# Kernel optimization log

Measured on AMD Instinct MI355X. Metric: run time of the kernel, lower is better.

## Reference

```python
import jax, jax.numpy as jnp
import numpy as np

FACTOR = 5  # sampling factor from __init__


def setup_inputs() -> dict:
    key = jax.random.key(0)
    k1, k2, k3, k4 = jax.random.split(key, 4)
    B, L, H, D = 4, 2048, 8, 64
    S = min(FACTOR * int(np.ceil(np.log(L))), L)  # U_part = 40
    return {
        "queries": jax.random.normal(k1, (B, L, H, D), jnp.float32),
        "keys": jax.random.normal(k2, (B, L, H, D), jnp.float32),
        "values": jax.random.normal(k3, (B, L, H, D), jnp.float32),
        "index_sample": jax.random.randint(k4, (L, S), 0, L, jnp.int32),
    }


def reference(queries, keys, values, index_sample):
    B, L_Q, H, D = queries.shape
    L_K = keys.shape[1]
    Q = jnp.transpose(queries, (0, 2, 1, 3))  # [B,H,L_Q,D]
    K = jnp.transpose(keys, (0, 2, 1, 3))     # [B,H,L_K,D]
    V = jnp.transpose(values, (0, 2, 1, 3))   # [B,H,L_K,D]

    u = min(FACTOR * int(np.ceil(np.log(L_Q))), L_Q)  # n_top

    # --- _prob_QK: sampled QK to score queries, then top-u query selection ---
    # K_sample[b,h,q,s,:] = K[b,h,index_sample[q,s],:]  -> [B,H,L_Q,S,D]
    K_sample = K[:, :, index_sample, :]
    Q_K_sample = jnp.einsum('bhqd,bhqsd->bhqs', Q, K_sample)  # [B,H,L_Q,S]
    M = Q_K_sample.max(-1) - Q_K_sample.sum(-1) / L_K         # sparsity measure
    _, M_top = jax.lax.top_k(M, u)                            # [B,H,u] query indices

    Q_reduce = jnp.take_along_axis(Q, M_top[..., None], axis=2)  # [B,H,u,D]
    scale = 1.0 / np.sqrt(D)
    scores = jnp.einsum('bhud,bhkd->bhuk', Q_reduce, K) * scale  # [B,H,u,L_K]

    # --- _update_context causal mask: rows are the FIRST u rows of the full
    # triu(L_Q,L_Q) mask (faithful to original, which does NOT reindex by M_top)
    causal = jnp.triu(jnp.ones((u, L_Q), dtype=bool), 1)
    scores = jnp.where(causal[None, None], -jnp.inf, scores)
    attn = jax.nn.softmax(scores, axis=-1)
    upd = jnp.einsum('bhuk,bhkd->bhud', attn, V)  # [B,H,u,D]

    # --- _get_initial_context (mask_flag=True): running cumsum of V ---
    context = jnp.cumsum(V, axis=2)  # [B,H,L_Q,D]

    # scatter-overwrite selected query positions
    b = jnp.arange(B)[:, None, None]
    h = jnp.arange(H)[None, :, None]
    context = context.at[b, h, M_top].set(upd)

    return jnp.transpose(context, (0, 2, 1, 3))  # [B,L_Q,H,D]
```

## Files before the change

kernel.cpp:

```cpp
#include <hip/hip_runtime.h>
#include <stdint.h>

constexpr int B = 4;
constexpr int L = 2048;
constexpr int H = 8;
constexpr int D = 64;
constexpr int S = 40;
constexpr int U = 40;
constexpr int HD = H * D;
constexpr int NSEG = 8;
constexpr int SEGL = L / NSEG;
constexpr int NC = 64;
constexpr int CL = L / NC;

__device__ __forceinline__ unsigned mono(float v) {
    unsigned u = __float_as_uint(v);
    return (u & 0x80000000u) ? ~u : (u | 0x80000000u);
}

__global__ __launch_bounds__(256) void k_scores(
    const float4* __restrict__ Q4, const float4* __restrict__ K4,
    const int* __restrict__ idxs, float* __restrict__ M)
{
    int i = blockIdx.x;
    int xcd = i & 7;
    int b = xcd >> 1;
    int qc = (i >> 3) * 2 + (xcd & 1);
    int w = threadIdx.x >> 6;
    int lane = threadIdx.x & 63;
    int q = qc * 4 + w;
    int h = lane >> 3;
    int dd = lane & 7;

    const float4* qrow = Q4 + (size_t)(b * L + q) * 128;
    float4 qa = qrow[2 * lane], qb = qrow[2 * lane + 1];

    int v_idx = idxs[q * S + (lane < S ? lane : 0)];

    const float4* kbase = K4 + (size_t)b * L * 128;
    float mx = -INFINITY, sm = 0.f;
    #pragma unroll 8
    for (int s = 0; s < S; ++s) {
        int ki = __shfl(v_idx, s);
        const float4* krow = kbase + (size_t)ki * 128;
        float4 ka = krow[2 * lane], kb = krow[2 * lane + 1];
        float d = qa.x * ka.x + qa.y * ka.y + qa.z * ka.z + qa.w * ka.w
                + qb.x * kb.x + qb.y * kb.y + qb.z * kb.z + qb.w * kb.w;
        d += __shfl_xor(d, 1);
        d += __shfl_xor(d, 2);
        d += __shfl_xor(d, 4);
        mx = fmaxf(mx, d);
        sm += d;
    }
    if (dd == 0)
        M[(b * 8 + h) * L + q] = mx - sm * (1.0f / (float)L);
}

__global__ __launch_bounds__(64) void k_seg_topk(
    const float* __restrict__ M, unsigned long long* __restrict__ cand,
    int* __restrict__ flags)
{
    int blk = blockIdx.x;
    int bh = blk >> 3, seg = blk & 7;
    int lane = threadIdx.x;
    int j0 = seg * SEGL + lane * 4;

    *(int4*)(flags + (size_t)bh * L + j0) = make_int4(0, 0, 0, 0);

    float4 v = *(const float4*)(M + (size_t)bh * L + j0);
    unsigned m[4] = { mono(v.x), mono(v.y), mono(v.z), mono(v.w) };
    int rank[4] = { 0, 0, 0, 0 };

    #pragma unroll 4
    for (int src = 0; src < 64; ++src) {
        #pragma unroll
        for (int slot = 0; slot < 4; ++slot) {
            unsigned bm = __shfl(m[slot], src);
            int bj = src * 4 + slot;
            #pragma unroll
            for (int s = 0; s < 4; ++s) {
                int myj = lane * 4 + s;
                rank[s] += (bm > m[s]) || (bm == m[s] && bj < myj);
            }
        }
    }

    unsigned long long* out = cand + (size_t)blk * U;
    #pragma unroll
    for (int s = 0; s < 4; ++s)
        if (rank[s] < U)
            out[rank[s]] = ((unsigned long long)m[s] << 32)
                         | (unsigned)(~(unsigned)(j0 + s));
}

__global__ __launch_bounds__(256) void k_attn(
    const float4* __restrict__ Q4, const float4* __restrict__ K4,
    const float4* __restrict__ V4, const unsigned long long* __restrict__ cand,
    int* __restrict__ flags, float* __restrict__ upd)
{
    __shared__ unsigned long long cnd[NSEG * U];
    __shared__ int top_idx[U];
    __shared__ __align__(16) float Qs[U * 68];
    __shared__ __align__(16) float Ks[U * 68];
    __shared__ __align__(16) float Vs[U * 68];
    __shared__ float P[U * 41];

    int bh = blockIdx.x;
    int b = bh >> 3, h = bh & 7;
    int tid = threadIdx.x;

    for (int i = tid; i < NSEG * U; i += 256)
        cnd[i] = cand[(size_t)bh * NSEG * U + i];
    __syncthreads();

    {
        unsigned long long ka = cnd[tid < NSEG * U ? tid : 0];
        unsigned long long kb = (tid < NSEG * U - 256) ? cnd[256 + tid] : 0ULL;
        int ra = 0, rb = 0;
        for (int j = 0; j < NSEG * U; ++j) {
            unsigned long long kj = cnd[j];
            ra += (kj > ka);
            rb += (kj > kb);
        }
        if (tid < NSEG * U && ra < U) top_idx[ra] = (int)(~(unsigned)ka);
        if (tid < NSEG * U - 256 && rb < U) top_idx[rb] = (int)(~(unsigned)kb);
    }
    __syncthreads();

    if (tid < U) flags[bh * L + top_idx[tid]] = tid + 1;

    for (int i = tid; i < U * 16; i += 256) {
        int r = i >> 4, d4 = i & 15;
        size_t kvbase = ((size_t)(b * L + r) * H + h) * 16 + d4;
        *(float4*)(Ks + r * 68 + d4 * 4) = K4[kvbase];
        *(float4*)(Vs + r * 68 + d4 * 4) = V4[kvbase];
        *(float4*)(Qs + r * 68 + d4 * 4) =
            Q4[((size_t)(b * L + top_idx[r]) * H + h) * 16 + d4];
    }
    __syncthreads();

    const float scale = 0.125f;
    for (int p = tid; p < U * U; p += 256) {
        int r = p / U, k = p - r * U;
        if (k <= r) {
            float acc = 0.f;
            #pragma unroll
            for (int d = 0; d < D; d += 4) {
                float4 a = *(const float4*)(Qs + r * 68 + d);
                float4 c = *(const float4*)(Ks + k * 68 + d);
                acc += a.x * c.x + a.y * c.y + a.z * c.z + a.w * c.w;
            }
            P[r * 41 + k] = acc * scale;
        }
    }
    __syncthreads();

    if (tid < U) {
        int r = tid;
        float mval = -INFINITY;
        for (int k = 0; k <= r; ++k) mval = fmaxf(mval, P[r * 41 + k]);
        float ssum = 0.f;
        for (int k = 0; k <= r; ++k) {
            float e = expf(P[r * 41 + k] - mval);
            P[r * 41 + k] = e;
            ssum += e;
        }
        float inv = 1.f / ssum;
        for (int k = 0; k <= r; ++k) P[r * 41 + k] *= inv;
    }
    __syncthreads();

    for (int t = tid; t < U * D; t += 256) {
        int r = t >> 6, d = t & 63;
        float acc = 0.f;
        for (int k = 0; k <= r; ++k) acc += P[r * 41 + k] * Vs[k * 68 + d];
        upd[((size_t)bh * U + r) * D + d] = acc;
    }
}

__global__ __launch_bounds__(512) void k_chunksum(
    const float* __restrict__ V, float* __restrict__ partial)
{
    int b = blockIdx.x >> 6;
    int c = blockIdx.x & 63;
    int hd = threadIdx.x;
    const float* vp = V + ((size_t)(b * L + c * CL)) * HD + hd;
    float s = 0.f;
    #pragma unroll
    for (int l = 0; l < CL; ++l) s += vp[(size_t)l * HD];
    partial[((size_t)b * NC + c) * HD + hd] = s;
}

__global__ __launch_bounds__(512) void k_scan(float* __restrict__ partial)
{
    int b = blockIdx.x;
    int hd = threadIdx.x;
    float acc = 0.f;
    #pragma unroll 8
    for (int c = 0; c < NC; ++c) {
        size_t o = ((size_t)b * NC + c) * HD + hd;
        float v = partial[o];
        partial[o] = acc;
        acc += v;
    }
}

__global__ __launch_bounds__(512) void k_cumsum_out(
    const float* __restrict__ V, const float* __restrict__ partial,
    const int* __restrict__ flags, const float* __restrict__ upd,
    float* __restrict__ out)
{
    int b = blockIdx.x >> 6;
    int c = blockIdx.x & 63;
    int hd = threadIdx.x;
    int h = hd >> 6, d = hd & 63;

    float acc = partial[((size_t)b * NC + c) * HD + hd];

    const float* vp = V + ((size_t)(b * L + c * CL)) * HD + hd;
    float*       op = out + ((size_t)(b * L + c * CL)) * HD + hd;
    const int*   fp = flags + (b * H + h) * L + c * CL;
    const float* up = upd + (size_t)(b * H + h) * U * D + d;

    #pragma unroll 4
    for (int l = 0; l < CL; ++l) {
        acc += vp[(size_t)l * HD];
        int f = fp[l];
        op[(size_t)l * HD] = f ? up[(size_t)(f - 1) * D] : acc;
    }
}

extern "C" void kernel_launch(void* const* d_in, const int* in_sizes, int n_in,
                              void* d_out, int out_size, void* d_ws, size_t ws_size,
                              hipStream_t stream)
{
    const float* Q   = (const float*)d_in[0];
    const float* K   = (const float*)d_in[1];
    const float* V   = (const float*)d_in[2];
    const int*  idxs = (const int*)d_in[3];
    float* out = (float*)d_out;

    char* ws = (char*)d_ws;
    float* M       = (float*)(ws);
    int*   flags   = (int*)  (ws + 262144);
    float* upd     = (float*)(ws + 524288);
    float* partial = (float*)(ws + 851968);
    unsigned long long* cand = (unsigned long long*)(ws + 1376256);

    k_scores    <<<B * L / 4,    256, 0, stream>>>((const float4*)Q, (const float4*)K, idxs, M);
    k_seg_topk  <<<B * H * NSEG,  64, 0, stream>>>(M, cand, flags);
    k_attn      <<<B * H,        256, 0, stream>>>((const float4*)Q, (const float4*)K, (const float4*)V,
                                                   cand, flags, upd);
    k_chunksum  <<<B * NC,       512, 0, stream>>>(V, partial);
    k_scan      <<<B,            512, 0, stream>>>(partial);
    k_cumsum_out<<<B * NC,       512, 0, stream>>>(V, partial, flags, upd, out);
}
```

Baseline: 174.3 us.

## Fuse all stages into one persistent kernel with software grid barriers

Replaces six kernel launches with a single 256-block persistent kernel that computes sampled scores and per-chunk V sums, synchronizes through a hand-rolled grid barrier, then has eight blocks per batch do top-k and the selected-query attention. A second barrier precedes the cumsum/scatter output pass. The chunk-offset scan is replaced by each block summing its preceding partials directly. This removes launch overhead and inter-kernel gaps, but leaves scoring spread over far fewer blocks and makes the attention stage use only 32 of 256 blocks. The barrier relies on all blocks being co-resident and on the slot counters being monotonic across calls, since they are never reset.

```diff
diff --git a/kernel.cpp b/kernel.cpp
--- a/kernel.cpp
+++ b/kernel.cpp
@@ -1,232 +1,206 @@
 #include <hip/hip_runtime.h>
 #include <stdint.h>
 
-constexpr int B = 4;
-constexpr int L = 2048;
-constexpr int H = 8;
-constexpr int D = 64;
-constexpr int S = 40;
-constexpr int U = 40;
+constexpr int B = 4, L = 2048, H = 8, D = 64, S = 40, U = 40;
 constexpr int HD = H * D;
-constexpr int NSEG = 8;
-constexpr int SEGL = L / NSEG;
 constexpr int NC = 64;
 constexpr int CL = L / NC;
+constexpr int NBLK = 256;
+constexpr int MAGIC = 1 << 30;
+constexpr int SLOTS = 16;
 
 __device__ __forceinline__ unsigned mono(float v) {
     unsigned u = __float_as_uint(v);
     return (u & 0x80000000u) ? ~u : (u | 0x80000000u);
 }
 
-__global__ __launch_bounds__(256) void k_scores(
+__device__ __forceinline__ void grid_barrier(int* slots, int bid, int phase) {
+    __syncthreads();
+    __threadfence();
+    if (threadIdx.x == 0)
+        atomicExch(&slots[bid * SLOTS], MAGIC + phase);
+    if (threadIdx.x < NBLK) {
+        while (atomicAdd(&slots[threadIdx.x * SLOTS], 0) < MAGIC + phase)
+            __builtin_amdgcn_s_sleep(8);
+    }
+    __threadfence();
+    __syncthreads();
+}
+
+__global__ __launch_bounds__(512) void k_fused(
     const float4* __restrict__ Q4, const float4* __restrict__ K4,
-    const int* __restrict__ idxs, float* __restrict__ M)
+    const float* __restrict__ V, const int* __restrict__ idxs,
+    float* __restrict__ Mg, int* __restrict__ flags, float* __restrict__ upd,
+    float* __restrict__ partial, int* __restrict__ slots, float* __restrict__ out)
 {
-    int i = blockIdx.x;
-    int xcd = i & 7;
-    int b = xcd >> 1;
-    int qc = (i >> 3) * 2 + (xcd & 1);
-    int w = threadIdx.x >> 6;
-    int lane = threadIdx.x & 63;
-    int q = qc * 4 + w;
-    int h = lane >> 3;
-    int dd = lane & 7;
-
-    const float4* qrow = Q4 + (size_t)(b * L + q) * 128;
-    float4 qa = qrow[2 * lane], qb = qrow[2 * lane + 1];
-
-    int v_idx = idxs[q * S + (lane < S ? lane : 0)];
-
-    const float4* kbase = K4 + (size_t)b * L * 128;
-    float mx = -INFINITY, sm = 0.f;
-    #pragma unroll 8
-    for (int s = 0; s < S; ++s) {
-        int ki = __shfl(v_idx, s);
-        const float4* krow = kbase + (size_t)ki * 128;
-        float4 ka = krow[2 * lane], kb = krow[2 * lane + 1];
-        float d = qa.x * ka.x + qa.y * ka.y + qa.z * ka.z + qa.w * ka.w
-                + qb.x * kb.x + qb.y * kb.y + qb.z * kb.z + qb.w * kb.w;
-        d += __shfl_xor(d, 1);
-        d += __shfl_xor(d, 2);
-        d += __shfl_xor(d, 4);
-        mx = fmaxf(mx, d);
-        sm += d;
-    }
-    if (dd == 0)
-        M[(b * 8 + h) * L + q] = mx - sm * (1.0f / (float)L);
-}
-
-__global__ __launch_bounds__(64) void k_seg_topk(
-    const float* __restrict__ M, unsigned long long* __restrict__ cand,
-    int* __restrict__ flags)
-{
-    int blk = blockIdx.x;
-    int bh = blk >> 3, seg = blk & 7;
-    int lane = threadIdx.x;
-    int j0 = seg * SEGL + lane * 4;
-
-    *(int4*)(flags + (size_t)bh * L + j0) = make_int4(0, 0, 0, 0);
-
-    float4 v = *(const float4*)(M + (size_t)bh * L + j0);
-    unsigned m[4] = { mono(v.x), mono(v.y), mono(v.z), mono(v.w) };
-    int rank[4] = { 0, 0, 0, 0 };
-
-    #pragma unroll 4
-    for (int src = 0; src < 64; ++src) {
-        #pragma unroll
-        for (int slot = 0; slot < 4; ++slot) {
-            unsigned bm = __shfl(m[slot], src);
-            int bj = src * 4 + slot;
-            #pragma unroll
-            for (int s = 0; s < 4; ++s) {
-                int myj = lane * 4 + s;
-                rank[s] += (bm > m[s]) || (bm == m[s] && bj < myj);
-            }
-        }
-    }
-
-    unsigned long long* out = cand + (size_t)blk * U;
-    #pragma unroll
-    for (int s = 0; s < 4; ++s)
-        if (rank[s] < U)
-            out[rank[s]] = ((unsigned long long)m[s] << 32)
-                         | (unsigned)(~(unsigned)(j0 + s));
-}
-
-__global__ __launch_bounds__(256) void k_attn(
-    const float4* __restrict__ Q4, const float4* __restrict__ K4,
-    const float4* __restrict__ V4, const unsigned long long* __restrict__ cand,
-    int* __restrict__ flags, float* __restrict__ upd)
-{
-    __shared__ unsigned long long cnd[NSEG * U];
+    __shared__ float4 Ms4[512];
+    __shared__ unsigned long long cnd[8 * U];
     __shared__ int top_idx[U];
     __shared__ __align__(16) float Qs[U * 68];
     __shared__ __align__(16) float Ks[U * 68];
     __shared__ __align__(16) float Vs[U * 68];
     __shared__ float P[U * 41];
 
-    int bh = blockIdx.x;
-    int b = bh >> 3, h = bh & 7;
+    int bid = blockIdx.x;
     int tid = threadIdx.x;
-
-    for (int i = tid; i < NSEG * U; i += 256)
-        cnd[i] = cand[(size_t)bh * NSEG * U + i];
-    __syncthreads();
+    int b   = (bid & 7) >> 1;
+    int sub = ((bid >> 3) << 1) | (bid & 1);
+    int c   = sub;
 
     {
-        unsigned long long ka = cnd[tid < NSEG * U ? tid : 0];
-        unsigned long long kb = (tid < NSEG * U - 256) ? cnd[256 + tid] : 0ULL;
-        int ra = 0, rb = 0;
-        for (int j = 0; j < NSEG * U; ++j) {
-            unsigned long long kj = cnd[j];
-            ra += (kj > ka);
-            rb += (kj > kb);
-        }
-        if (tid < NSEG * U && ra < U) top_idx[ra] = (int)(~(unsigned)ka);
-        if (tid < NSEG * U - 256 && rb < U) top_idx[rb] = (int)(~(unsigned)kb);
-    }
-    __syncthreads();
-
-    if (tid < U) flags[bh * L + top_idx[tid]] = tid + 1;
-
-    for (int i = tid; i < U * 16; i += 256) {
-        int r = i >> 4, d4 = i & 15;
-        size_t kvbase = ((size_t)(b * L + r) * H + h) * 16 + d4;
-        *(float4*)(Ks + r * 68 + d4 * 4) = K4[kvbase];
-        *(float4*)(Vs + r * 68 + d4 * 4) = V4[kvbase];
-        *(float4*)(Qs + r * 68 + d4 * 4) =
-            Q4[((size_t)(b * L + top_idx[r]) * H + h) * 16 + d4];
-    }
-    __syncthreads();
-
-    const float scale = 0.125f;
-    for (int p = tid; p < U * U; p += 256) {
-        int r = p / U, k = p - r * U;
-        if (k <= r) {
+        int w = tid >> 6, lane = tid & 63;
+        int dd = lane & 7;
+        for (int j = 0; j < 4; ++j) {
+            int q = sub * 32 + w * 4 + j;
+            const float4* qrow = Q4 + (size_t)(b * L + q) * 128;
+            float4 qa = qrow[2 * lane], qb = qrow[2 * lane + 1];
+            int v_idx = idxs[q * S + (lane < S ? lane : 0)];
+            float mx = -INFINITY, sm = 0.f;
+            #pragma unroll 8
+            for (int s = 0; s < S; ++s) {
+                int ki = __shfl(v_idx, s);
+                const float4* krow = K4 + (size_t)(b * L + ki) * 128;
+                float4 ka = krow[2 * lane], kb = krow[2 * lane + 1];
+                float dt = qa.x * ka.x + qa.y * ka.y + qa.z * ka.z + qa.w * ka.w
+                         + qb.x * kb.x + qb.y * kb.y + qb.z * kb.z + qb.w * kb.w;
+                dt += __shfl_xor(dt, 1);
+                dt += __shfl_xor(dt, 2);
+                dt += __shfl_xor(dt, 4);
+                mx = fmaxf(mx, dt);
+                sm += dt;
+            }
+            if (dd == 0) {
+                int h = lane >> 3;
+                Mg[(size_t)(b * 8 + h) * L + q] = mx - sm * (1.0f / (float)L);
+            }
+        }
+    }
+    {
+        const float* vp = V + ((size_t)(b * L + c * CL)) * HD + tid;
+        float s = 0.f;
+        #pragma unroll
+        for (int l = 0; l < CL; ++l) s += vp[(size_t)l * HD];
+        partial[((size_t)b * NC + c) * HD + tid] = s;
+    }
+    if (tid < 256) {
+        int h = tid >> 5, l0 = c * CL + (tid & 31);
+        flags[(size_t)(b * 8 + h) * L + l0] = 0;
+    }
+
+    grid_barrier(slots, bid, 1);
+
+    if (sub < 8) {
+        int h = sub, bh = b * 8 + h;
+        Ms4[tid] = ((const float4*)(Mg + (size_t)bh * L))[tid];
+        __syncthreads();
+
+        {
+            int w = tid >> 6, lane = tid & 63;
+            float4 v = Ms4[w * 64 + lane];
+            unsigned m[4] = { mono(v.x), mono(v.y), mono(v.z), mono(v.w) };
+            int rank[4] = { 0, 0, 0, 0 };
+            #pragma unroll 4
+            for (int src = 0; src < 64; ++src) {
+                #pragma unroll
+                for (int slot = 0; slot < 4; ++slot) {
+                    unsigned bm = __shfl(m[slot], src);
+                    int bj = src * 4 + slot;
+                    #pragma unroll
+                    for (int s2 = 0; s2 < 4; ++s2) {
+                        int myj = lane * 4 + s2;
+                        rank[s2] += (bm > m[s2]) || (bm == m[s2] && bj < myj);
+                    }
+                }
+            }
+            int j0 = w * 256 + lane * 4;
+            #pragma unroll
+            for (int s2 = 0; s2 < 4; ++s2)
+                if (rank[s2] < U)
+                    cnd[w * U + rank[s2]] = ((unsigned long long)m[s2] << 32)
+                                          | (unsigned)(~(unsigned)(j0 + s2));
+        }
+        __syncthreads();
+
+        if (tid < 8 * U) {
+            unsigned long long ka = cnd[tid];
+            int ra = 0;
+            for (int j = 0; j < 8 * U; ++j) ra += (cnd[j] > ka);
+            if (ra < U) {
+                int qi = (int)(~(unsigned)ka);
+                top_idx[ra] = qi;
+                flags[(size_t)bh * L + qi] = ra + 1;
+            }
+        }
+        __syncthreads();
+
+        const float4* V4 = (const float4*)V;
+        for (int i2 = tid; i2 < U * 16; i2 += 512) {
+            int r = i2 >> 4, d4 = i2 & 15;
+            size_t kvb = (size_t)(b * L + r) * 128 + h * 16 + d4;
+            *(float4*)(Ks + r * 68 + d4 * 4) = K4[kvb];
+            *(float4*)(Vs + r * 68 + d4 * 4) = V4[kvb];
+            *(float4*)(Qs + r * 68 + d4 * 4) =
+                Q4[(size_t)(b * L + top_idx[r]) * 128 + h * 16 + d4];
+        }
+        __syncthreads();
+
+        const float scale = 0.125f;
+        for (int p = tid; p < U * U; p += 512) {
+            int r = p / U, k = p - r * U;
+            if (k <= r) {
+                float acc = 0.f;
+                #pragma unroll
+                for (int d = 0; d < D; d += 4) {
+                    float4 a = *(const float4*)(Qs + r * 68 + d);
+                    float4 cc = *(const float4*)(Ks + k * 68 + d);
+                    acc += a.x * cc.x + a.y * cc.y + a.z * cc.z + a.w * cc.w;
+                }
+                P[r * 41 + k] = acc * scale;
+            }
+        }
+        __syncthreads();
+
+        if (tid < U) {
+            int r = tid;
+            float mval = -INFINITY;
+            for (int k = 0; k <= r; ++k) mval = fmaxf(mval, P[r * 41 + k]);
+            float ssum = 0.f;
+            for (int k = 0; k <= r; ++k) {
+                float e = expf(P[r * 41 + k] - mval);
+                P[r * 41 + k] = e;
+                ssum += e;
+            }
+            float inv = 1.f / ssum;
+            for (int k = 0; k <= r; ++k) P[r * 41 + k] *= inv;
+        }
+        __syncthreads();
+
+        for (int t = tid; t < U * D; t += 512) {
+            int r = t >> 6, d = t & 63;
             float acc = 0.f;
-            #pragma unroll
-            for (int d = 0; d < D; d += 4) {
-                float4 a = *(const float4*)(Qs + r * 68 + d);
-                float4 c = *(const float4*)(Ks + k * 68 + d);
-                acc += a.x * c.x + a.y * c.y + a.z * c.z + a.w * c.w;
-            }
-            P[r * 41 + k] = acc * scale;
-        }
-    }
-    __syncthreads();
-
-    if (tid < U) {
-        int r = tid;
-        float mval = -INFINITY;
-        for (int k = 0; k <= r; ++k) mval = fmaxf(mval, P[r * 41 + k]);
-        float ssum = 0.f;
-        for (int k = 0; k <= r; ++k) {
-            float e = expf(P[r * 41 + k] - mval);
-            P[r * 41 + k] = e;
-            ssum += e;
-        }
-        float inv = 1.f / ssum;
-        for (int k = 0; k <= r; ++k) P[r * 41 + k] *= inv;
-    }
-    __syncthreads();
-
-    for (int t = tid; t < U * D; t += 256) {
-        int r = t >> 6, d = t & 63;
-        float acc = 0.f;
-        for (int k = 0; k <= r; ++k) acc += P[r * 41 + k] * Vs[k * 68 + d];
-        upd[((size_t)bh * U + r) * D + d] = acc;
-    }
-}
-
-__global__ __launch_bounds__(512) void k_chunksum(
-    const float* __restrict__ V, float* __restrict__ partial)
-{
-    int b = blockIdx.x >> 6;
-    int c = blockIdx.x & 63;
-    int hd = threadIdx.x;
-    const float* vp = V + ((size_t)(b * L + c * CL)) * HD + hd;
-    float s = 0.f;
-    #pragma unroll
-    for (int l = 0; l < CL; ++l) s += vp[(size_t)l * HD];
-    partial[((size_t)b * NC + c) * HD + hd] = s;
-}
-
-__global__ __launch_bounds__(512) void k_scan(float* __restrict__ partial)
-{
-    int b = blockIdx.x;
-    int hd = threadIdx.x;
+            for (int k = 0; k <= r; ++k) acc += P[r * 41 + k] * Vs[k * 68 + d];
+            upd[((size_t)bh * U + r) * D + d] = acc;
+        }
+    }
+
     float acc = 0.f;
-    #pragma unroll 8
-    for (int c = 0; c < NC; ++c) {
-        size_t o = ((size_t)b * NC + c) * HD + hd;
-        float v = partial[o];
-        partial[o] = acc;
-        acc += v;
-    }
-}
-
-__global__ __launch_bounds__(512) void k_cumsum_out(
-    const float* __restrict__ V, const float* __restrict__ partial,
-    const int* __restrict__ flags, const float* __restrict__ upd,
-    float* __restrict__ out)
-{
-    int b = blockIdx.x >> 6;
-    int c = blockIdx.x & 63;
-    int hd = threadIdx.x;
-    int h = hd >> 6, d = hd & 63;
-
-    float acc = partial[((size_t)b * NC + c) * HD + hd];
-
-    const float* vp = V + ((size_t)(b * L + c * CL)) * HD + hd;
-    float*       op = out + ((size_t)(b * L + c * CL)) * HD + hd;
-    const int*   fp = flags + (b * H + h) * L + c * CL;
-    const float* up = upd + (size_t)(b * H + h) * U * D + d;
-
-    #pragma unroll 4
-    for (int l = 0; l < CL; ++l) {
-        acc += vp[(size_t)l * HD];
-        int f = fp[l];
-        op[(size_t)l * HD] = f ? up[(size_t)(f - 1) * D] : acc;
+    for (int cc = 0; cc < c; ++cc)
+        acc += partial[((size_t)b * NC + cc) * HD + tid];
+
+    grid_barrier(slots, bid, 2);
+
+    {
+        int h = tid >> 6, d = tid & 63;
+        const float* vp = V + ((size_t)(b * L + c * CL)) * HD + tid;
+        float*       op = out + ((size_t)(b * L + c * CL)) * HD + tid;
+        const int*   fp = flags + (size_t)(b * 8 + h) * L + c * CL;
+        const float* up = upd + (size_t)(b * 8 + h) * U * D + d;
+        #pragma unroll 4
+        for (int l = 0; l < CL; ++l) {
+            acc += vp[(size_t)l * HD];
+            int f = fp[l];
+            op[(size_t)l * HD] = f ? up[(size_t)(f - 1) * D] : acc;
+        }
     }
 }
 
@@ -241,17 +215,12 @@
     float* out = (float*)d_out;
 
     char* ws = (char*)d_ws;
-    float* M       = (float*)(ws);
+    float* Mg      = (float*)(ws);
     int*   flags   = (int*)  (ws + 262144);
     float* upd     = (float*)(ws + 524288);
     float* partial = (float*)(ws + 851968);
-    unsigned long long* cand = (unsigned long long*)(ws + 1376256);
-
-    k_scores    <<<B * L / 4,    256, 0, stream>>>((const float4*)Q, (const float4*)K, idxs, M);
-    k_seg_topk  <<<B * H * NSEG,  64, 0, stream>>>(M, cand, flags);
-    k_attn      <<<B * H,        256, 0, stream>>>((const float4*)Q, (const float4*)K, (const float4*)V,
-                                                   cand, flags, upd);
-    k_chunksum  <<<B * NC,       512, 0, stream>>>(V, partial);
-    k_scan      <<<B,            512, 0, stream>>>(partial);
-    k_cumsum_out<<<B * NC,       512, 0, stream>>>(V, partial, flags, upd, out);
-}
+    int*   slots   = (int*)  (ws + 1376256);
+
+    k_fused<<<NBLK, 512, 0, stream>>>((const float4*)Q, (const float4*)K, V, idxs,
+                                      Mg, flags, upd, partial, slots, out);
+}
```

Measured after the change: 278.0 us. 1.59x slower.
